# Optimization experiments

Hardware: AMD Instinct MI355X
Metric: run time of the kernel (lower is better)

The kernel has to match this reference:

```python
import jax, jax.numpy as jnp
import numpy as np

HIDDEN = 768
HEADS = 12
HEAD_DIM = HIDDEN // HEADS  # 64


def setup_inputs() -> dict:
    key = jax.random.key(0)
    k1, k2, k3 = jax.random.split(key, 3)
    B, N, C = 64, 197, HIDDEN
    hidden_states = jax.random.normal(k1, (B, N, C), dtype=jnp.float32)
    # qkv Linear: weight [C, 3C] (stored transposed for x @ W), bias [3C]
    w_qkv = jax.random.normal(k2, (C, 3 * C), dtype=jnp.float32) * (1.0 / np.sqrt(C))
    b_qkv = jax.random.normal(k3, (3 * C,), dtype=jnp.float32) * 0.02
    return {"hidden_states": hidden_states, "w_qkv": w_qkv, "b_qkv": b_qkv}


def reference(hidden_states, w_qkv, b_qkv):
    B, N, C = hidden_states.shape
    scale = HEAD_DIM ** -0.5
    qkv = hidden_states @ w_qkv + b_qkv                      # [B, N, 3C]
    qkv = qkv.reshape(B, N, 3, HEADS, HEAD_DIM)
    qkv = jnp.transpose(qkv, (2, 0, 3, 1, 4))                # [3, B, H, N, d]
    q, k, v = qkv[0], qkv[1], qkv[2]
    scores = jnp.einsum("bhqd,bhkd->bhqk", q, k) * scale     # [B, H, N, N]
    probs = jax.nn.softmax(scores, axis=-1)
    # dropout is identity in eval mode (p=0.0)
    ctx = jnp.einsum("bhqk,bhkd->bhqd", probs, v)            # [B, H, N, d]
    ctx = jnp.transpose(ctx, (0, 2, 1, 3)).reshape(B, N, C)  # [B, N, C]
    return ctx
```

## Files before the change

### kernel.cpp

```cpp
#include <hip/hip_runtime.h>

#define M_ROWS 12608
#define K_DIM  768
#define XC_ELEMS (64*24*16*512)
#define WC_ELEMS (12*24*12*512)

typedef __bf16 bf16x8 __attribute__((ext_vector_type(8)));
typedef float  f32x4  __attribute__((ext_vector_type(4)));

__device__ __forceinline__ unsigned short f2bf(float f) {
    unsigned u = __builtin_bit_cast(unsigned, f);
    u += 0x7fffu + ((u >> 16) & 1u);
    return (unsigned short)(u >> 16);
}

__device__ __forceinline__ void gll16(const unsigned short* g, unsigned short* l) {
    __builtin_amdgcn_global_load_lds(
        (const __attribute__((address_space(1))) unsigned int*)g,
        (__attribute__((address_space(3))) unsigned int*)l, 16, 0, 0);
}

__global__ __launch_bounds__(256) void prep_kernel(
        const float* __restrict__ X, unsigned short* __restrict__ Xc,
        const float* __restrict__ W, unsigned short* __restrict__ Wc) {
    __shared__ float tile[32][33];
    const int bid = blockIdx.x;
    const int t = threadIdx.x;
    if (bid < 6144) {
        const int cg = bid * 4 + (t >> 6);
        const int lane = t & 63;
        const int p = cg / 384, rem = cg - p * 384;
        const int kt = rem >> 4, c = rem & 15;
        const int kc = c >> 2, rg = c & 3;
        const int grow = p * 197 + rg * 64 + lane;
        uint4 u = (uint4){0, 0, 0, 0};
        if (grow < M_ROWS) {
            const float* src = X + (size_t)grow * K_DIM + kt * 32 + kc * 8;
            float4 a = *(const float4*)src;
            float4 b = *(const float4*)(src + 4);
            u.x = f2bf(a.x) | ((unsigned)f2bf(a.y) << 16);
            u.y = f2bf(a.z) | ((unsigned)f2bf(a.w) << 16);
            u.z = f2bf(b.x) | ((unsigned)f2bf(b.y) << 16);
            u.w = f2bf(b.z) | ((unsigned)f2bf(b.w) << 16);
        }
        *(uint4*)(Xc + (size_t)cg * 512 + lane * 8) = u;
        return;
    }
    const int b2 = bid - 6144;
    const int n0 = (b2 % 72) * 32, k0 = (b2 / 72) * 32;
    const int tx = t & 31, ty = t >> 5;
#pragma unroll
    for (int i = 0; i < 4; ++i)
        tile[ty + i * 8][tx] = W[(size_t)(k0 + ty + i * 8) * 2304 + n0 + tx];
    __syncthreads();
    if (t < 128) {
        const int kc = t >> 5, tx2 = t & 31;
        const int grp = n0 / 768, remn = n0 - grp * 768;
        const int h = remn >> 6, lh = remn & 63;
        const int kt = k0 >> 5;
        uint4 u;
        u.x = f2bf(tile[kc * 8 + 0][tx2]) | ((unsigned)f2bf(tile[kc * 8 + 1][tx2]) << 16);
        u.y = f2bf(tile[kc * 8 + 2][tx2]) | ((unsigned)f2bf(tile[kc * 8 + 3][tx2]) << 16);
        u.z = f2bf(tile[kc * 8 + 4][tx2]) | ((unsigned)f2bf(tile[kc * 8 + 5][tx2]) << 16);
        u.w = f2bf(tile[kc * 8 + 6][tx2]) | ((unsigned)f2bf(tile[kc * 8 + 7][tx2]) << 16);
        *(uint4*)(Wc + (size_t)(((h * 24 + kt) * 12) + kc * 3 + grp) * 512 + (lh + tx2) * 8) = u;
    }
}

__global__ __launch_bounds__(512, 2) void fused_kernel(
        const unsigned short* __restrict__ Xc, const unsigned short* __restrict__ Wc,
        const float* __restrict__ bias, float* __restrict__ out) {
    __shared__ __align__(16) unsigned short L[70864];

    const int t = threadIdx.x;
    const int w = t >> 6, lane = t & 63, quad = lane >> 4, l16 = lane & 15;
    const int wrow0 = (w >> 1) * 64;
    const int wcol0 = (w & 1) * 96;

    const int lin = blockIdx.x;
    const int wg = (lin & 7) * 96 + (lin >> 3);
    const int bb = wg / 12, h = wg - bb * 12;

    const unsigned short* sgp[4];
    int sof[4];
    const int nst = (w < 4) ? 4 : 3;
    const int bstride = (w < 4) ? 8192 : 6144;
    const int kstride = (w < 4) ? 8192 : 6144;
    if (w < 4) {
#pragma unroll
        for (int s = 0; s < 4; ++s) {
            sgp[s] = Xc + ((size_t)(bb * 24) * 16 + w * 4 + s) * 512 + lane * 8;
            sof[s] = (w * 4 + s) * 512;
        }
    } else {
#pragma unroll
        for (int s = 0; s < 3; ++s) {
            const int idx = (w - 4) * 3 + s;
            const int kc = idx & 3, grp = idx >> 2;
            sgp[s] = Wc + ((size_t)(h * 24) * 12 + kc * 3 + grp) * 512 + lane * 8;
            sof[s] = 16384 + (kc * 3 + grp) * 512;
        }
        sgp[3] = sgp[0]; sof[3] = sof[0];
    }

    f32x4 acc[4][6];
#pragma unroll
    for (int i = 0; i < 4; ++i)
#pragma unroll
        for (int j = 0; j < 6; ++j) acc[i][j] = (f32x4){0.f, 0.f, 0.f, 0.f};

#pragma unroll
    for (int s = 0; s < 4; ++s)
        if (s < nst) gll16(sgp[s], &L[sof[s]]);
    asm volatile("s_waitcnt vmcnt(0)" ::: "memory");
    __builtin_amdgcn_s_barrier();
    asm volatile("" ::: "memory");

#pragma unroll 2
    for (int kt = 0; kt < 24; ++kt) {
        const int cur = kt & 1, nxt = cur ^ 1;
        const int sk = (kt + 1 < 24 ? kt + 1 : 0) * kstride;

#pragma unroll
        for (int s = 0; s < 4; ++s)
            if (s < nst) gll16(sgp[s] + sk, &L[sof[s] + nxt * bstride]);

        const unsigned short* Ab = &L[cur * 8192];
        const unsigned short* Bb = &L[16384 + cur * 6144];
        bf16x8 af[4], bq[6];
#pragma unroll
        for (int i = 0; i < 4; ++i)
            af[i] = *(const bf16x8*)&Ab[quad * 2048 + (wrow0 + i * 16 + l16) * 8];
#pragma unroll
        for (int j = 0; j < 6; ++j)
            bq[j] = *(const bf16x8*)&Bb[quad * 1536 + (wcol0 + j * 16 + l16) * 8];

#pragma unroll
        for (int i = 0; i < 4; ++i)
#pragma unroll
            for (int j = 0; j < 6; ++j)
                acc[i][j] = __builtin_amdgcn_mfma_f32_16x16x32_bf16(af[i], bq[j], acc[i][j], 0, 0, 0);

        asm volatile("s_waitcnt vmcnt(0)" ::: "memory");
        __builtin_amdgcn_s_barrier();
        asm volatile("" ::: "memory");
    }

    unsigned short* Qs = &L[28672];
    unsigned short* Ks = &L[42856];
    unsigned short* Vt = &L[57040];
    unsigned short* Ps = &L[0];

#pragma unroll
    for (int j = 0; j < 6; ++j) {
        const int gnr = wcol0 + j * 16 + l16;
        const int which = gnr >> 6, d = gnr & 63;
        const float bv = bias[which * 768 + h * 64 + d];
#pragma unroll
        for (int i = 0; i < 4; ++i) {
            const int rowb = wrow0 + i * 16 + quad * 4;
#pragma unroll
            for (int r = 0; r < 4; ++r) {
                const int row = rowb + r;
                if (row >= 197) continue;
                const float val = acc[i][j][r] + bv;
                if (which == 0)      Qs[row * 72 + d] = f2bf(val * 0.125f);
                else if (which == 1) Ks[row * 72 + d] = f2bf(val);
                else                 Vt[d * 216 + row] = f2bf(val);
            }
        }
    }
    for (int idx = t; idx < 64 * 19; idx += 512) {
        int d = idx / 19, c = 197 + idx - d * 19;
        Vt[d * 216 + c] = 0;
    }
    __syncthreads();

    unsigned short* Pw = Ps + w * (16 * 136);

    for (int tile = w; tile < 13; tile += 8) {
        int rq = tile * 16 + l16;
        int tokq = rq < 197 ? rq : 196;
        bf16x8 aq0 = *(const bf16x8*)&Qs[tokq * 72 + quad * 8];
        bf16x8 aq1 = *(const bf16x8*)&Qs[tokq * 72 + 32 + quad * 8];

        f32x4 s[13];
        __builtin_amdgcn_s_setprio(1);
#pragma unroll
        for (int c = 0; c < 13; ++c) {
            int krow = c * 16 + l16;
            if (krow > 196) krow = 196;
            bf16x8 kb0 = *(const bf16x8*)&Ks[krow * 72 + quad * 8];
            bf16x8 kb1 = *(const bf16x8*)&Ks[krow * 72 + 32 + quad * 8];
            f32x4 zz = (f32x4){0.f, 0.f, 0.f, 0.f};
            zz = __builtin_amdgcn_mfma_f32_16x16x32_bf16(aq0, kb0, zz, 0, 0, 0);
            zz = __builtin_amdgcn_mfma_f32_16x16x32_bf16(aq1, kb1, zz, 0, 0, 0);
            s[c] = zz;
        }
        __builtin_amdgcn_s_setprio(0);
        if (l16 >= 5) { s[12][0] = -1e30f; s[12][1] = -1e30f; s[12][2] = -1e30f; s[12][3] = -1e30f; }

        float mx[4], lsum[4];
#pragma unroll
        for (int r = 0; r < 4; ++r) {
            float m = s[0][r];
#pragma unroll
            for (int c = 1; c < 13; ++c) m = fmaxf(m, s[c][r]);
#pragma unroll
            for (int d = 1; d < 16; d <<= 1) m = fmaxf(m, __shfl_xor(m, d));
            mx[r] = m;
            lsum[r] = 0.f;
        }
#pragma unroll
        for (int c = 0; c < 13; ++c)
#pragma unroll
            for (int r = 0; r < 4; ++r) {
                float p = __expf(s[c][r] - mx[r]);
                s[c][r] = p;
                lsum[r] += p;
            }
#pragma unroll
        for (int r = 0; r < 4; ++r)
#pragma unroll
            for (int d = 1; d < 16; d <<= 1) lsum[r] += __shfl_xor(lsum[r], d);

        f32x4 o[4];
#pragma unroll
        for (int j = 0; j < 4; ++j) o[j] = (f32x4){0.f, 0.f, 0.f, 0.f};

#pragma unroll
        for (int c = 0; c < 8; ++c)
#pragma unroll
            for (int r = 0; r < 4; ++r)
                Pw[(quad * 4 + r) * 136 + c * 16 + l16] = f2bf(s[c][r]);
        __builtin_amdgcn_s_setprio(1);
#pragma unroll
        for (int kc = 0; kc < 4; ++kc) {
            int kof = kc * 32 + quad * 8;
            bf16x8 ap = *(const bf16x8*)&Pw[l16 * 136 + kof];
#pragma unroll
            for (int j = 0; j < 4; ++j) {
                bf16x8 bv = *(const bf16x8*)&Vt[(j * 16 + l16) * 216 + kof];
                o[j] = __builtin_amdgcn_mfma_f32_16x16x32_bf16(ap, bv, o[j], 0, 0, 0);
            }
        }
        __builtin_amdgcn_s_setprio(0);
#pragma unroll
        for (int r = 0; r < 4; ++r)
            Pw[(quad * 4 + r) * 136 + 80 + l16] = 0;
#pragma unroll
        for (int c = 8; c < 13; ++c)
#pragma unroll
            for (int r = 0; r < 4; ++r)
                Pw[(quad * 4 + r) * 136 + (c - 8) * 16 + l16] = f2bf(s[c][r]);
        __builtin_amdgcn_s_setprio(1);
#pragma unroll
        for (int kc = 0; kc < 3; ++kc) {
            int kofA = kc * 32 + quad * 8;
            int kofB = (kc == 2 && quad >= 2) ? 0 : kofA;
            bf16x8 ap = *(const bf16x8*)&Pw[l16 * 136 + kofA];
#pragma unroll
            for (int j = 0; j < 4; ++j) {
                bf16x8 bv = *(const bf16x8*)&Vt[(j * 16 + l16) * 216 + 128 + kofB];
                o[j] = __builtin_amdgcn_mfma_f32_16x16x32_bf16(ap, bv, o[j], 0, 0, 0);
            }
        }
        __builtin_amdgcn_s_setprio(0);

        int tokbase = tile * 16 + quad * 4;
#pragma unroll
        for (int r = 0; r < 4; ++r) {
            int tr = tokbase + r;
            if (tr >= 197) continue;
            float inv = 1.f / lsum[r];
#pragma unroll
            for (int j = 0; j < 4; ++j)
                out[((size_t)(bb * 197 + tr)) * 768 + h * 64 + j * 16 + l16] = o[j][r] * inv;
        }
    }
}

extern "C" void kernel_launch(void* const* d_in, const int* in_sizes, int n_in,
                              void* d_out, int out_size, void* d_ws, size_t ws_size,
                              hipStream_t stream) {
    const float* X    = (const float*)d_in[0];
    const float* W    = (const float*)d_in[1];
    const float* bias = (const float*)d_in[2];
    float* out = (float*)d_out;

    unsigned short* Xc = (unsigned short*)d_ws;
    unsigned short* Wc = (unsigned short*)d_ws + XC_ELEMS;

    prep_kernel<<<7872, 256, 0, stream>>>(X, Xc, W, Wc);
    fused_kernel<<<768, 512, 0, stream>>>(Xc, Wc, bias, out);
}
```

Before: 201.2 us.

## Use 12 waves per block with a 4x3 wave tiling of the QKV GEMM

Raises the fused kernel's block from 512 to 768 threads. The per-head QKV GEMM is split into a 4x3 grid of 64x64 wave tiles, replacing the 4x2 grid of 64x96 tiles, and the global-to-LDS load slots are redistributed across the 12 waves. The LDS layout is reshuffled so the per-wave P buffers fit, and the attention tiles are spread over 12 waves. The aim is more waves per CU to hide latency and fewer MFMAs per wave in the GEMM. The cost is more VGPR pressure per wave, and the 13 attention tiles still leave one wave doing two.

```diff
diff --git a/kernel.cpp b/kernel.cpp
--- a/kernel.cpp
+++ b/kernel.cpp
@@ -67,50 +67,50 @@
     }
 }
 
-__global__ __launch_bounds__(512, 2) void fused_kernel(
+__global__ __launch_bounds__(768) void fused_kernel(
         const unsigned short* __restrict__ Xc, const unsigned short* __restrict__ Wc,
         const float* __restrict__ bias, float* __restrict__ out) {
-    __shared__ __align__(16) unsigned short L[70864];
+    __shared__ __align__(16) unsigned short L[68304];
 
     const int t = threadIdx.x;
     const int w = t >> 6, lane = t & 63, quad = lane >> 4, l16 = lane & 15;
-    const int wrow0 = (w >> 1) * 64;
-    const int wcol0 = (w & 1) * 96;
+    const int wr = w >> 2, wn = w & 3;
+    const int wm = w / 3, wnn = w - wm * 3;
+    const int wrow0 = wm * 64;
+    const int wcol0 = wnn * 64;
+    (void)wr; (void)wn;
 
     const int lin = blockIdx.x;
     const int wg = (lin & 7) * 96 + (lin >> 3);
     const int bb = wg / 12, h = wg - bb * 12;
 
-    const unsigned short* sgp[4];
-    int sof[4];
-    const int nst = (w < 4) ? 4 : 3;
-    const int bstride = (w < 4) ? 8192 : 6144;
-    const int kstride = (w < 4) ? 8192 : 6144;
-    if (w < 4) {
-#pragma unroll
-        for (int s = 0; s < 4; ++s) {
-            sgp[s] = Xc + ((size_t)(bb * 24) * 16 + w * 4 + s) * 512 + lane * 8;
-            sof[s] = (w * 4 + s) * 512;
-        }
-    } else {
+    const unsigned short* sgp[3];
+    int sof[3], gst[3], bst[3];
+    const int nst = (w < 4) ? 3 : 2;
+    {
+        const int clist[3] = {w, w + 12, 24 + w};
 #pragma unroll
         for (int s = 0; s < 3; ++s) {
-            const int idx = (w - 4) * 3 + s;
-            const int kc = idx & 3, grp = idx >> 2;
-            sgp[s] = Wc + ((size_t)(h * 24) * 12 + kc * 3 + grp) * 512 + lane * 8;
-            sof[s] = 16384 + (kc * 3 + grp) * 512;
-        }
-        sgp[3] = sgp[0]; sof[3] = sof[0];
-    }
-
-    f32x4 acc[4][6];
+            const int c = clist[s];
+            if (c < 16) {
+                sgp[s] = Xc + ((size_t)bb * 384 + c) * 512 + lane * 8;
+                sof[s] = c * 512; gst[s] = 8192; bst[s] = 8192;
+            } else {
+                const int cb = c - 16;
+                sgp[s] = Wc + ((size_t)h * 288 + cb) * 512 + lane * 8;
+                sof[s] = 16384 + cb * 512; gst[s] = 6144; bst[s] = 6144;
+            }
+        }
+    }
+
+    f32x4 acc[4][4];
 #pragma unroll
     for (int i = 0; i < 4; ++i)
 #pragma unroll
-        for (int j = 0; j < 6; ++j) acc[i][j] = (f32x4){0.f, 0.f, 0.f, 0.f};
-
-#pragma unroll
-    for (int s = 0; s < 4; ++s)
+        for (int j = 0; j < 4; ++j) acc[i][j] = (f32x4){0.f, 0.f, 0.f, 0.f};
+
+#pragma unroll
+    for (int s = 0; s < 3; ++s)
         if (s < nst) gll16(sgp[s], &L[sof[s]]);
     asm volatile("s_waitcnt vmcnt(0)" ::: "memory");
     __builtin_amdgcn_s_barrier();
@@ -119,26 +119,26 @@
 #pragma unroll 2
     for (int kt = 0; kt < 24; ++kt) {
         const int cur = kt & 1, nxt = cur ^ 1;
-        const int sk = (kt + 1 < 24 ? kt + 1 : 0) * kstride;
-
-#pragma unroll
-        for (int s = 0; s < 4; ++s)
-            if (s < nst) gll16(sgp[s] + sk, &L[sof[s] + nxt * bstride]);
+        const int skt = (kt + 1 < 24 ? kt + 1 : 0);
+
+#pragma unroll
+        for (int s = 0; s < 3; ++s)
+            if (s < nst) gll16(sgp[s] + (size_t)skt * gst[s], &L[sof[s] + nxt * bst[s]]);
 
         const unsigned short* Ab = &L[cur * 8192];
         const unsigned short* Bb = &L[16384 + cur * 6144];
-        bf16x8 af[4], bq[6];
+        bf16x8 af[4], bq[4];
 #pragma unroll
         for (int i = 0; i < 4; ++i)
             af[i] = *(const bf16x8*)&Ab[quad * 2048 + (wrow0 + i * 16 + l16) * 8];
 #pragma unroll
-        for (int j = 0; j < 6; ++j)
+        for (int j = 0; j < 4; ++j)
             bq[j] = *(const bf16x8*)&Bb[quad * 1536 + (wcol0 + j * 16 + l16) * 8];
 
 #pragma unroll
         for (int i = 0; i < 4; ++i)
 #pragma unroll
-            for (int j = 0; j < 6; ++j)
+            for (int j = 0; j < 4; ++j)
                 acc[i][j] = __builtin_amdgcn_mfma_f32_16x16x32_bf16(af[i], bq[j], acc[i][j], 0, 0, 0);
 
         asm volatile("s_waitcnt vmcnt(0)" ::: "memory");
@@ -146,31 +146,33 @@
         asm volatile("" ::: "memory");
     }
 
-    unsigned short* Qs = &L[28672];
-    unsigned short* Ks = &L[42856];
-    unsigned short* Vt = &L[57040];
-    unsigned short* Ps = &L[0];
-
-#pragma unroll
-    for (int j = 0; j < 6; ++j) {
-        const int gnr = wcol0 + j * 16 + l16;
-        const int which = gnr >> 6, d = gnr & 63;
-        const float bv = bias[which * 768 + h * 64 + d];
-#pragma unroll
-        for (int i = 0; i < 4; ++i) {
-            const int rowb = wrow0 + i * 16 + quad * 4;
-#pragma unroll
-            for (int r = 0; r < 4; ++r) {
-                const int row = rowb + r;
-                if (row >= 197) continue;
-                const float val = acc[i][j][r] + bv;
-                if (which == 0)      Qs[row * 72 + d] = f2bf(val * 0.125f);
-                else if (which == 1) Ks[row * 72 + d] = f2bf(val);
-                else                 Vt[d * 216 + row] = f2bf(val);
-            }
-        }
-    }
-    for (int idx = t; idx < 64 * 19; idx += 512) {
+    unsigned short* Qs = &L[0];
+    unsigned short* Ks = &L[14184];
+    unsigned short* Vt = &L[28368];
+    unsigned short* Ps = &L[42192];
+
+    {
+        const float bscale = (wnn == 0) ? 0.125f : 1.0f;
+#pragma unroll
+        for (int j = 0; j < 4; ++j) {
+            const int d = j * 16 + l16;
+            const float bv = bias[wnn * 768 + h * 64 + d];
+#pragma unroll
+            for (int i = 0; i < 4; ++i) {
+                const int rowb = wrow0 + i * 16 + quad * 4;
+#pragma unroll
+                for (int r = 0; r < 4; ++r) {
+                    const int row = rowb + r;
+                    if (row >= 197) continue;
+                    const float val = (acc[i][j][r] + bv) * bscale;
+                    if (wnn == 0)      Qs[row * 72 + d] = f2bf(val);
+                    else if (wnn == 1) Ks[row * 72 + d] = f2bf(val);
+                    else               Vt[d * 216 + row] = f2bf(val);
+                }
+            }
+        }
+    }
+    for (int idx = t; idx < 64 * 19; idx += 768) {
         int d = idx / 19, c = 197 + idx - d * 19;
         Vt[d * 216 + c] = 0;
     }
@@ -178,7 +180,7 @@
 
     unsigned short* Pw = Ps + w * (16 * 136);
 
-    for (int tile = w; tile < 13; tile += 8) {
+    for (int tile = w; tile < 13; tile += 12) {
         int rq = tile * 16 + l16;
         int tokq = rq < 197 ? rq : 196;
         bf16x8 aq0 = *(const bf16x8*)&Qs[tokq * 72 + quad * 8];
@@ -292,5 +294,5 @@
     unsigned short* Wc = (unsigned short*)d_ws + XC_ELEMS;
 
     prep_kernel<<<7872, 256, 0, stream>>>(X, Xc, W, Wc);
-    fused_kernel<<<768, 512, 0, stream>>>(Xc, Wc, bias, out);
-}
+    fused_kernel<<<768, 768, 0, stream>>>(Xc, Wc, bias, out);
+}
```

Measured after the change: 203.0 us. Within noise of the previous version (+0.9%).
